# Optimization experiments

Measured on AMD Instinct MI355X. Metric: run time of the kernel, lower is better.

The kernel has to match this reference:

```python
import jax, jax.numpy as jnp
import numpy as np

NUM_HEADS = 16
THETA = 10000.0


def _rope(x):
    # x: [b, h, s, d_k], interleaved-pair RoPE
    s, d = x.shape[-2], x.shape[-1]
    inv_freq = 1.0 / (THETA ** (jnp.arange(0, d, 2, dtype=jnp.float32) / d))  # [d/2]
    ang = jnp.arange(s, dtype=jnp.float32)[:, None] * inv_freq[None, :]       # [s, d/2]
    cos = jnp.repeat(jnp.cos(ang), 2, axis=-1)[None, None]                    # [1,1,s,d]
    sin = jnp.repeat(jnp.sin(ang), 2, axis=-1)[None, None]
    x_even = x[..., 0::2]
    x_odd = x[..., 1::2]
    rot = jnp.stack((-x_odd, x_even), axis=-1).reshape(x.shape)
    return x * cos.astype(x.dtype) + rot * sin.astype(x.dtype)


def setup_inputs() -> dict:
    key = jax.random.key(0)
    ks = jax.random.split(key, 5)
    b, s, d = 4, 2048, 1024
    std = (2.0 / (d + d)) ** 0.5
    return {
        "x": jax.random.normal(ks[0], (b, s, d), dtype=jnp.float32),
        "wq": jax.random.normal(ks[1], (d, d), dtype=jnp.float32) * std,
        "wk": jax.random.normal(ks[2], (d, d), dtype=jnp.float32) * std,
        "wv": jax.random.normal(ks[3], (d, d), dtype=jnp.float32) * std,
        "wo": jax.random.normal(ks[4], (d, d), dtype=jnp.float32) * std,
    }


def reference(x, wq, wk, wv, wo):
    b, s, d_model = x.shape
    h = NUM_HEADS
    d_k = d_model // h

    def proj(w):
        y = jnp.einsum('bsd,od->bso', x, w)
        return y.reshape(b, s, h, d_k).transpose(0, 2, 1, 3)  # [b,h,s,d_k]

    q = _rope(proj(wq))
    k = _rope(proj(wk))
    v = proj(wv)

    scores = jnp.einsum('bhqd,bhkd->bhqk', q, k) / (d_k ** 0.5)
    causal = jnp.tril(jnp.ones((s, s), dtype=bool))[None, None]
    scores = jnp.where(causal, scores, -jnp.inf)
    attn = jax.nn.softmax(scores, axis=-1)
    out = jnp.einsum('bhqk,bhkd->bhqd', attn, v)
    out = out.transpose(0, 2, 1, 3).reshape(b, s, d_model)
    return jnp.einsum('bsd,od->bso', out, wo)
```

## Files before the change

### kernel.cpp

```cpp
#include <hip/hip_runtime.h>
#include <stdint.h>

#define NHEAD  16
#define SEQ    2048
#define DMODEL 1024
#define BATCH  4

typedef __attribute__((ext_vector_type(4))) float f32x4;
typedef __attribute__((ext_vector_type(8))) __bf16 bf16x8;
typedef __attribute__((ext_vector_type(8))) unsigned short u16x8;

__device__ __forceinline__ unsigned short f2bf(float f) {
    unsigned int u = __builtin_bit_cast(unsigned int, f);
    u += 0x7FFFu + ((u >> 16) & 1u);
    return (unsigned short)(u >> 16);
}

__device__ __forceinline__ unsigned int cvt_pk_bf16(float lo, float hi) {
    unsigned int r;
    asm("v_cvt_pk_bf16_f32 %0, %1, %2" : "=v"(r) : "v"(lo), "v"(hi));
    return r;
}

__device__ __forceinline__ void gload_lds16(const void* g, void* l) {
    __builtin_amdgcn_global_load_lds(
        (const __attribute__((address_space(1))) unsigned int*)(uintptr_t)g,
        (__attribute__((address_space(3))) unsigned int*)(uintptr_t)l,
        16, 0, 0);
}

__device__ __forceinline__ bf16x8 lds_frag(const unsigned short* p) {
    return __builtin_bit_cast(bf16x8, *(const u16x8*)p);
}

__device__ __forceinline__ bf16x8 gfrag(const unsigned short* p) {
    return __builtin_bit_cast(bf16x8, *(const u16x8*)p);
}

__global__ __launch_bounds__(256) void cvt_f32_bf16(const float* __restrict__ src,
                                                    unsigned short* __restrict__ dst, int n4) {
    int i = blockIdx.x * 256 + threadIdx.x;
    if (i < n4) {
        float4 v = ((const float4*)src)[i];
        ushort4 o;
        o.x = f2bf(v.x); o.y = f2bf(v.y); o.z = f2bf(v.z); o.w = f2bf(v.w);
        ((ushort4*)dst)[i] = o;
    }
}

__global__ __launch_bounds__(256) void cvt_weights(const float* __restrict__ w0,
                                                   const float* __restrict__ w1,
                                                   const float* __restrict__ w2,
                                                   const float* __restrict__ w3,
                                                   unsigned short* __restrict__ dst) {
    int which = blockIdx.x >> 10;
    int i = (blockIdx.x & 1023) * 256 + threadIdx.x;
    const float* src = which == 0 ? w0 : which == 1 ? w1 : which == 2 ? w2 : w3;
    unsigned short* d = dst + (size_t)which * 1024 * 1024;
    float4 v = ((const float4*)src)[i];
    ushort4 o;
    o.x = f2bf(v.x); o.y = f2bf(v.y); o.z = f2bf(v.z); o.w = f2bf(v.w);
    ((ushort4*)d)[i] = o;
}

__global__ __launch_bounds__(256) void gemm_qkv(const unsigned short* __restrict__ A,
                                                const unsigned short* __restrict__ Wc,
                                                unsigned short* __restrict__ qw,
                                                unsigned short* __restrict__ kw,
                                                unsigned short* __restrict__ vw) {
    __shared__ __align__(16) unsigned short As[2][128 * 64];
    __shared__ __align__(16) unsigned short Bs[2][128 * 64];

    const int tid  = threadIdx.x;
    const int lane = tid & 63;
    const int wid  = tid >> 6;
    const int wm = wid >> 1, wn = wid & 1;
    const int l15 = lane & 15, lg = lane >> 4;

    const int tn = blockIdx.x;
    const int m0 = blockIdx.y * 128, n0 = tn * 128;

    f32x4 acc[4][4];
#pragma unroll
    for (int i = 0; i < 4; i++)
#pragma unroll
        for (int j = 0; j < 4; j++) acc[i][j] = f32x4{0.f, 0.f, 0.f, 0.f};

    const int e0 = tid * 8;
    auto STAGE = [&](int kk, int bufi) {
#pragma unroll
        for (int is = 0; is < 4; ++is) {
            int e = is * 2048 + e0;
            int row = e >> 6, col = e & 63;
            gload_lds16(A  + (size_t)(m0 + row) * 1024 + kk + col, &As[bufi][e]);
            gload_lds16(Wc + (size_t)(n0 + row) * 1024 + kk + col, &Bs[bufi][e]);
        }
    };

    STAGE(0, 0);
    __syncthreads();

    for (int kk = 0; kk < 1024; kk += 64) {
        const int cur = (kk >> 6) & 1;
        if (kk + 64 < 1024) STAGE(kk + 64, cur ^ 1);
#pragma unroll
        for (int ks = 0; ks < 2; ++ks) {
            bf16x8 a[4], b[4];
#pragma unroll
            for (int f = 0; f < 4; f++) {
                a[f] = lds_frag(&As[cur][(wm * 64 + f * 16 + l15) * 64 + ks * 32 + lg * 8]);
                b[f] = lds_frag(&Bs[cur][(wn * 64 + f * 16 + l15) * 64 + ks * 32 + lg * 8]);
            }
#pragma unroll
            for (int i = 0; i < 4; i++)
#pragma unroll
                for (int j = 0; j < 4; j++)
                    acc[i][j] = __builtin_amdgcn_mfma_f32_16x16x32_bf16(a[i], b[j], acc[i][j], 0, 0, 0);
        }
        __syncthreads();
    }

    if (tn >= 16) {
        unsigned short* out = vw;
#pragma unroll
        for (int i = 0; i < 4; i++)
#pragma unroll
            for (int r = 0; r < 4; r++) {
                int m = m0 + wm * 64 + i * 16 + lg * 4 + r;
                int b = m >> 11, s = m & 2047;
#pragma unroll
                for (int j = 0; j < 4; j++) {
                    int n = n0 + wn * 64 + j * 16 + l15;
                    int h = (n >> 6) & 15, dk = n & 63;
                    out[((size_t)(b * NHEAD + h) * 64 + dk) * SEQ + s] = f2bf(acc[i][j][r]);
                }
            }
    } else {
        unsigned short* out = (tn < 8) ? qw : kw;
        const float qscale = (tn < 8) ? 0.18033688011112042f : 1.0f;
        const float L2T = 13.287712379549449f;
        float invf[4];
#pragma unroll
        for (int j = 0; j < 4; j++) {
            int idx = j * 16 + l15;
            int t = idx >> 1;
            invf[j] = exp2f(-((float)(2 * t) * (1.0f / 64.0f)) * L2T);
        }
        const int par = l15 & 1;
#pragma unroll
        for (int i = 0; i < 4; i++)
#pragma unroll
            for (int r = 0; r < 4; r++) {
                int m = m0 + wm * 64 + i * 16 + lg * 4 + r;
                int b = m >> 11, s = m & 2047;
                float fs = (float)s;
#pragma unroll
                for (int j = 0; j < 4; j++) {
                    float v = acc[i][j][r];
                    float other = __shfl_xor(v, 1);
                    float sn, cs;
                    __sincosf(fs * invf[j], &sn, &cs);
                    float y = par ? fmaf(v, cs, other * sn) : fmaf(v, cs, -other * sn);
                    y *= qscale;
                    int n = n0 + wn * 64 + j * 16 + l15;
                    int h = (n >> 6) & 15, dk = n & 63;
                    out[((size_t)(b * NHEAD + h) * SEQ + s) * 64 + dk] = f2bf(y);
                }
            }
    }
}

__global__ __launch_bounds__(256) void gemm_out(const unsigned short* __restrict__ A,
                                                const unsigned short* __restrict__ W,
                                                float* __restrict__ out) {
    __shared__ __align__(16) unsigned short As[2][128 * 64];
    __shared__ __align__(16) unsigned short Bs[2][128 * 64];

    const int tid  = threadIdx.x;
    const int lane = tid & 63;
    const int wid  = tid >> 6;
    const int wm = wid >> 1, wn = wid & 1;
    const int l15 = lane & 15, lg = lane >> 4;

    const int tn = blockIdx.x & 7;
    const int tm = blockIdx.x >> 3;
    const int m0 = tm * 128, n0 = tn * 128;

    f32x4 acc[4][4];
#pragma unroll
    for (int i = 0; i < 4; i++)
#pragma unroll
        for (int j = 0; j < 4; j++) acc[i][j] = f32x4{0.f, 0.f, 0.f, 0.f};

    const int e0 = tid * 8;
    auto STAGE = [&](int kk, int bufi) {
#pragma unroll
        for (int is = 0; is < 4; ++is) {
            int e = is * 2048 + e0;
            int row = e >> 6, col = e & 63;
            gload_lds16(A + (size_t)(m0 + row) * 1024 + kk + col, &As[bufi][e]);
            gload_lds16(W + (size_t)(n0 + row) * 1024 + kk + col, &Bs[bufi][e]);
        }
    };

    STAGE(0, 0);
    __syncthreads();

    for (int kk = 0; kk < 1024; kk += 64) {
        const int cur = (kk >> 6) & 1;
        if (kk + 64 < 1024) STAGE(kk + 64, cur ^ 1);
#pragma unroll
        for (int ks = 0; ks < 2; ++ks) {
            bf16x8 a[4], b[4];
#pragma unroll
            for (int f = 0; f < 4; f++) {
                a[f] = lds_frag(&As[cur][(wm * 64 + f * 16 + l15) * 64 + ks * 32 + lg * 8]);
                b[f] = lds_frag(&Bs[cur][(wn * 64 + f * 16 + l15) * 64 + ks * 32 + lg * 8]);
            }
#pragma unroll
            for (int i = 0; i < 4; i++)
#pragma unroll
                for (int j = 0; j < 4; j++)
                    acc[i][j] = __builtin_amdgcn_mfma_f32_16x16x32_bf16(a[i], b[j], acc[i][j], 0, 0, 0);
        }
        __syncthreads();
    }

#pragma unroll
    for (int i = 0; i < 4; i++)
#pragma unroll
        for (int r = 0; r < 4; r++) {
            int m = m0 + wm * 64 + i * 16 + lg * 4 + r;
            float* orow = out + (size_t)m * 1024 + n0 + wn * 64 + l15;
#pragma unroll
            for (int j = 0; j < 4; j++) orow[j * 16] = acc[i][j][r];
        }
}

__global__ __launch_bounds__(256, 4) void flash_attn(const unsigned short* __restrict__ Qw,
                                                     const unsigned short* __restrict__ Kw,
                                                     const unsigned short* __restrict__ Vw,
                                                     unsigned short* __restrict__ Ow) {
    __shared__ __align__(16) unsigned short Ks[2][64 * 64];
    __shared__ __align__(16) unsigned short Vs[2][64 * 64];
    __shared__ __align__(16) unsigned short Ps[64 * 64];

    const int tid  = threadIdx.x;
    const int lane = tid & 63;
    const int w    = tid >> 6;
    const int l15 = lane & 15, lg = lane >> 4;
    const int l7 = l15 & 7;

    const int logical = (blockIdx.x & 7) * 128 + (blockIdx.x >> 3);
    const int bh = logical >> 4;
    const int p  = logical & 15;
    const int qbB = 31 - p;
    const int ktmax = qbB;

    const unsigned short* Kbh = Kw + (size_t)bh * (SEQ * 64);
    const unsigned short* Vbh = Vw + (size_t)bh * (64 * SEQ);

    const int qrow0 = w * 16;
    const int prow  = qrow0 + l15;

    const unsigned short* QrowA = Qw + (size_t)bh * (SEQ * 64) + (size_t)(p * 64 + prow) * 64;
    const unsigned short* QrowB = Qw + (size_t)bh * (SEQ * 64) + (size_t)(qbB * 64 + prow) * 64;
    bf16x8 qA0 = gfrag(QrowA + lg * 8), qA1 = gfrag(QrowA + 32 + lg * 8);
    bf16x8 qB0 = gfrag(QrowB + lg * 8), qB1 = gfrag(QrowB + 32 + lg * 8);

    auto STAGE = [&](int kt2, int bufi) {
#pragma unroll
        for (int is = 0; is < 2; ++is) {
            int e = (is * 256 + tid) * 8;
            int row = e >> 6, c = (e >> 3) & 7;
            int sc = (c ^ (row & 7)) << 3;
            gload_lds16(Kbh + (size_t)kt2 * 4096 + row * 64 + sc, &Ks[bufi][e]);
            gload_lds16(Vbh + (size_t)row * SEQ + kt2 * 64 + sc, &Vs[bufi][e]);
        }
    };

    STAGE(0, 0);

    f32x4 oaccA[4], oaccB[4];
#pragma unroll
    for (int f = 0; f < 4; f++) { oaccA[f] = f32x4{0.f, 0.f, 0.f, 0.f}; oaccB[f] = f32x4{0.f, 0.f, 0.f, 0.f}; }
    float mA = -3.0e38f, lA = 0.f, mB = -3.0e38f, lB = 0.f;

    unsigned short* pbase = &Ps[prow * 64];
    const unsigned short* prd = &Ps[prow * 64];

    __syncthreads();

    for (int kt = 0; kt <= ktmax; ++kt) {
        const int cur = kt & 1;
        if (kt < ktmax) STAGE(kt + 1, cur ^ 1);

        auto PROC = [&](bf16x8 q0, bf16x8 q1, f32x4* oacc, float& mrun, float& lrun, bool diag) {
            f32x4 st[4];
#pragma unroll
            for (int f = 0; f < 4; f++) st[f] = f32x4{0.f, 0.f, 0.f, 0.f};
            __builtin_amdgcn_s_setprio(1);
#pragma unroll
            for (int ks = 0; ks < 2; ++ks) {
                bf16x8 qk = (ks == 0) ? q0 : q1;
#pragma unroll
                for (int f = 0; f < 4; f++) {
                    bf16x8 kfrag = lds_frag(&Ks[cur][(f * 16 + l15) * 64 + (((ks * 4 + lg) ^ l7) << 3)]);
                    st[f] = __builtin_amdgcn_mfma_f32_16x16x32_bf16(kfrag, qk, st[f], 0, 0, 0);
                }
            }
            __builtin_amdgcn_s_setprio(0);

            if (diag) {
#pragma unroll
                for (int f = 0; f < 4; f++)
#pragma unroll
                    for (int r = 0; r < 4; r++) {
                        int kv = f * 16 + 4 * lg + r;
                        if (kv > prow) st[f][r] = -3.0e38f;
                    }
            }

            float pm = fmaxf(fmaxf(fmaxf(st[0][0], st[0][1]), fmaxf(st[0][2], st[0][3])),
                             fmaxf(fmaxf(st[1][0], st[1][1]), fmaxf(st[1][2], st[1][3])));
            pm = fmaxf(pm, fmaxf(fmaxf(fmaxf(st[2][0], st[2][1]), fmaxf(st[2][2], st[2][3])),
                                 fmaxf(fmaxf(st[3][0], st[3][1]), fmaxf(st[3][2], st[3][3]))));
            pm = fmaxf(pm, __shfl_xor(pm, 16));
            pm = fmaxf(pm, __shfl_xor(pm, 32));

            if (!__all(pm - mrun <= 8.0f)) {
                float mnew = fmaxf(mrun, pm);
                float sc0 = exp2f(mrun - mnew);
                mrun = mnew;
                lrun *= sc0;
#pragma unroll
                for (int r = 0; r < 4; r++) {
                    float so = __shfl(sc0, lg * 4 + r);
#pragma unroll
                    for (int f = 0; f < 4; f++) oacc[f][r] *= so;
                }
            }

            float lsum = 0.f;
#pragma unroll
            for (int f = 0; f < 4; f++)
#pragma unroll
                for (int r = 0; r < 4; r++) {
                    float e = exp2f(st[f][r] - mrun);
                    st[f][r] = e;
                    lsum += e;
                }
            lsum += __shfl_xor(lsum, 16);
            lsum += __shfl_xor(lsum, 32);
            lrun += lsum;

            {
                const int halfoff = (lg & 1) << 2;
                const int cbase = lg >> 1;
#pragma unroll
                for (int f = 0; f < 4; f++) {
                    uint2 pw;
                    pw.x = cvt_pk_bf16(st[f][0], st[f][1]);
                    pw.y = cvt_pk_bf16(st[f][2], st[f][3]);
                    *(uint2*)(pbase + (((2 * f + cbase) ^ l7) << 3) + halfoff) = pw;
                }
            }

            __builtin_amdgcn_s_setprio(1);
#pragma unroll
            for (int ks = 0; ks < 2; ++ks) {
                bf16x8 pa = lds_frag(prd + (((ks * 4 + lg) ^ l7) << 3));
#pragma unroll
                for (int f = 0; f < 4; f++) {
                    bf16x8 vb = lds_frag(&Vs[cur][(f * 16 + l15) * 64 + (((ks * 4 + lg) ^ l7) << 3)]);
                    oacc[f] = __builtin_amdgcn_mfma_f32_16x16x32_bf16(pa, vb, oacc[f], 0, 0, 0);
                }
            }
            __builtin_amdgcn_s_setprio(0);
        };

        if (kt <= p) PROC(qA0, qA1, oaccA, mA, lA, kt == p);
        PROC(qB0, qB1, oaccB, mB, lB, kt == ktmax);

        __syncthreads();
    }

    const int b = bh >> 4, h = bh & 15;
#pragma unroll
    for (int r = 0; r < 4; r++) {
        float lrA = __shfl(lA, lg * 4 + r);
        float invA = 1.0f / lrA;
        int sgA = p * 64 + qrow0 + lg * 4 + r;
        unsigned short* orowA = Ow + ((size_t)(b * SEQ + sgA) * DMODEL) + h * 64 + l15;
#pragma unroll
        for (int f = 0; f < 4; f++) orowA[f * 16] = f2bf(oaccA[f][r] * invA);

        float lrB = __shfl(lB, lg * 4 + r);
        float invB = 1.0f / lrB;
        int sgB = qbB * 64 + qrow0 + lg * 4 + r;
        unsigned short* orowB = Ow + ((size_t)(b * SEQ + sgB) * DMODEL) + h * 64 + l15;
#pragma unroll
        for (int f = 0; f < 4; f++) orowB[f * 16] = f2bf(oaccB[f][r] * invB);
    }
}

extern "C" void kernel_launch(void* const* d_in, const int* in_sizes, int n_in,
                              void* d_out, int out_size, void* d_ws, size_t ws_size,
                              hipStream_t stream) {
    const float* x  = (const float*)d_in[0];
    const float* wq = (const float*)d_in[1];
    const float* wk = (const float*)d_in[2];
    const float* wv = (const float*)d_in[3];
    const float* wo = (const float*)d_in[4];

    unsigned short* ws = (unsigned short*)d_ws;
    const size_t MEL = (size_t)8192 * 1024;
    const size_t WEL = (size_t)1024 * 1024;
    unsigned short* xb  = ws;
    unsigned short* wqb = xb + MEL;
    unsigned short* wob = wqb + 3 * WEL;
    unsigned short* qw  = wob + WEL;
    unsigned short* kw  = qw + MEL;
    unsigned short* vw  = kw + MEL;
    unsigned short* ow  = vw + MEL;

    cvt_f32_bf16<<<8192, 256, 0, stream>>>(x, xb, (int)(MEL / 4));
    cvt_weights<<<4096, 256, 0, stream>>>(wq, wk, wv, wo, wqb);

    gemm_qkv<<<dim3(24, 64), 256, 0, stream>>>(xb, wqb, qw, kw, vw);

    flash_attn<<<1024, 256, 0, stream>>>(qw, kw, vw, ow);

    gemm_out<<<512, 256, 0, stream>>>(ow, wob, (float*)d_out);
}
```

Before: 190.0 us.

## Unify QKV and output GEMMs into 256x128 tile triple-buffered swizzled kernel

Result: slower. 197.4 us (+3.9%).

```diff
diff --git a/kernel.cpp b/kernel.cpp
--- a/kernel.cpp
+++ b/kernel.cpp
@@ -63,22 +63,48 @@
     ((ushort4*)d)[i] = o;
 }
 
-__global__ __launch_bounds__(256) void gemm_qkv(const unsigned short* __restrict__ A,
-                                                const unsigned short* __restrict__ Wc,
-                                                unsigned short* __restrict__ qw,
-                                                unsigned short* __restrict__ kw,
-                                                unsigned short* __restrict__ vw) {
-    __shared__ __align__(16) unsigned short As[2][128 * 64];
-    __shared__ __align__(16) unsigned short Bs[2][128 * 64];
+template <int MODE>
+__global__ __launch_bounds__(512, 1) void gemm256(const unsigned short* __restrict__ A,
+                                                  const unsigned short* __restrict__ Wc,
+                                                  unsigned short* __restrict__ qw,
+                                                  unsigned short* __restrict__ kw,
+                                                  unsigned short* __restrict__ vw,
+                                                  float* __restrict__ fout) {
+    extern __shared__ __align__(16) unsigned short lds[];
+    unsigned short* As = lds;
+    unsigned short* Bs = lds + 3 * 16384;
 
     const int tid  = threadIdx.x;
     const int lane = tid & 63;
     const int wid  = tid >> 6;
     const int wm = wid >> 1, wn = wid & 1;
     const int l15 = lane & 15, lg = lane >> 4;
+    const int l7 = l15 & 7;
 
     const int tn = blockIdx.x;
-    const int m0 = blockIdx.y * 128, n0 = tn * 128;
+    const int m0 = blockIdx.y * 256, n0 = tn * 128;
+
+    auto STAGE_A = [&](int kt, int buf, int is) {
+        int e = (is * 512 + tid) * 8;
+        int row = e >> 6, c = (e >> 3) & 7;
+        gload_lds16(A + (size_t)(m0 + row) * 1024 + kt * 64 + ((c ^ (row & 7)) << 3),
+                    &As[buf * 16384 + e]);
+    };
+    auto STAGE_B = [&](int kt, int buf, int is) {
+        int e = (is * 512 + tid) * 8;
+        int row = e >> 6, c = (e >> 3) & 7;
+        gload_lds16(Wc + (size_t)(n0 + row) * 1024 + kt * 64 + ((c ^ (row & 7)) << 3),
+                    &Bs[buf * 8192 + e]);
+    };
+
+#pragma unroll
+    for (int is = 0; is < 4; ++is) STAGE_A(0, 0, is);
+#pragma unroll
+    for (int is = 0; is < 2; ++is) STAGE_B(0, 0, is);
+#pragma unroll
+    for (int is = 0; is < 4; ++is) STAGE_A(1, 1, is);
+#pragma unroll
+    for (int is = 0; is < 2; ++is) STAGE_B(1, 1, is);
 
     f32x4 acc[4][4];
 #pragma unroll
@@ -86,41 +112,79 @@
 #pragma unroll
         for (int j = 0; j < 4; j++) acc[i][j] = f32x4{0.f, 0.f, 0.f, 0.f};
 
-    const int e0 = tid * 8;
-    auto STAGE = [&](int kk, int bufi) {
-#pragma unroll
-        for (int is = 0; is < 4; ++is) {
-            int e = is * 2048 + e0;
-            int row = e >> 6, col = e & 63;
-            gload_lds16(A  + (size_t)(m0 + row) * 1024 + kk + col, &As[bufi][e]);
-            gload_lds16(Wc + (size_t)(n0 + row) * 1024 + kk + col, &Bs[bufi][e]);
-        }
-    };
-
-    STAGE(0, 0);
-    __syncthreads();
-
-    for (int kk = 0; kk < 1024; kk += 64) {
-        const int cur = (kk >> 6) & 1;
-        if (kk + 64 < 1024) STAGE(kk + 64, cur ^ 1);
-#pragma unroll
-        for (int ks = 0; ks < 2; ++ks) {
+    const int aoff = (wm * 64 + l15) * 64;
+    const int boff = (wn * 64 + l15) * 64;
+    const int c0 = (lg ^ l7) << 3;
+    const int c1 = ((4 + lg) ^ l7) << 3;
+
+    for (int kt = 0; kt < 16; ++kt) {
+        const int buf  = kt % 3;
+        const int buf2 = (kt + 2) % 3;
+        const unsigned short* Ab = As + buf * 16384;
+        const unsigned short* Bb = Bs + buf * 8192;
+
+        if (kt < 15) asm volatile("s_waitcnt vmcnt(6)" ::: "memory");
+        else         asm volatile("s_waitcnt vmcnt(0)" ::: "memory");
+        __builtin_amdgcn_sched_barrier(0);
+        __builtin_amdgcn_s_barrier();
+
+        if (kt + 2 < 16) {
+            STAGE_A(kt + 2, buf2, 0);
+            STAGE_A(kt + 2, buf2, 1);
+            STAGE_A(kt + 2, buf2, 2);
+        }
+        {
             bf16x8 a[4], b[4];
 #pragma unroll
-            for (int f = 0; f < 4; f++) {
-                a[f] = lds_frag(&As[cur][(wm * 64 + f * 16 + l15) * 64 + ks * 32 + lg * 8]);
-                b[f] = lds_frag(&Bs[cur][(wn * 64 + f * 16 + l15) * 64 + ks * 32 + lg * 8]);
-            }
+            for (int i = 0; i < 4; i++) a[i] = lds_frag(Ab + aoff + i * 1024 + c0);
+#pragma unroll
+            for (int n = 0; n < 4; n++) b[n] = lds_frag(Bb + boff + n * 1024 + c0);
+            asm volatile("s_waitcnt lgkmcnt(0)" ::: "memory");
+            __builtin_amdgcn_sched_barrier(0);
+            __builtin_amdgcn_s_setprio(1);
 #pragma unroll
             for (int i = 0; i < 4; i++)
 #pragma unroll
-                for (int j = 0; j < 4; j++)
-                    acc[i][j] = __builtin_amdgcn_mfma_f32_16x16x32_bf16(a[i], b[j], acc[i][j], 0, 0, 0);
-        }
-        __syncthreads();
+                for (int n = 0; n < 4; n++)
+                    acc[i][n] = __builtin_amdgcn_mfma_f32_16x16x32_bf16(a[i], b[n], acc[i][n], 0, 0, 0);
+            __builtin_amdgcn_s_setprio(0);
+        }
+
+        if (kt + 2 < 16) {
+            STAGE_A(kt + 2, buf2, 3);
+            STAGE_B(kt + 2, buf2, 0);
+            STAGE_B(kt + 2, buf2, 1);
+        }
+        {
+            bf16x8 a[4], b[4];
+#pragma unroll
+            for (int i = 0; i < 4; i++) a[i] = lds_frag(Ab + aoff + i * 1024 + c1);
+#pragma unroll
+            for (int n = 0; n < 4; n++) b[n] = lds_frag(Bb + boff + n * 1024 + c1);
+            asm volatile("s_waitcnt lgkmcnt(0)" ::: "memory");
+            __builtin_amdgcn_sched_barrier(0);
+            __builtin_amdgcn_s_setprio(1);
+#pragma unroll
+            for (int i = 0; i < 4; i++)
+#pragma unroll
+                for (int n = 0; n < 4; n++)
+                    acc[i][n] = __builtin_amdgcn_mfma_f32_16x16x32_bf16(a[i], b[n], acc[i][n], 0, 0, 0);
+            __builtin_amdgcn_s_setprio(0);
+        }
     }
 
-    if (tn >= 16) {
+    if (MODE == 1) {
+        float* out = fout;
+#pragma unroll
+        for (int i = 0; i < 4; i++)
+#pragma unroll
+            for (int r = 0; r < 4; r++) {
+                int m = m0 + wm * 64 + i * 16 + lg * 4 + r;
+                float* orow = out + (size_t)m * 1024 + n0 + wn * 64 + l15;
+#pragma unroll
+                for (int j = 0; j < 4; j++) orow[j * 16] = acc[i][j][r];
+            }
+    } else if (tn >= 16) {
         unsigned short* out = vw;
 #pragma unroll
         for (int i = 0; i < 4; i++)
@@ -170,73 +234,6 @@
     }
 }
 
-__global__ __launch_bounds__(256) void gemm_out(const unsigned short* __restrict__ A,
-                                                const unsigned short* __restrict__ W,
-                                                float* __restrict__ out) {
-    __shared__ __align__(16) unsigned short As[2][128 * 64];
-    __shared__ __align__(16) unsigned short Bs[2][128 * 64];
-
-    const int tid  = threadIdx.x;
-    const int lane = tid & 63;
-    const int wid  = tid >> 6;
-    const int wm = wid >> 1, wn = wid & 1;
-    const int l15 = lane & 15, lg = lane >> 4;
-
-    const int tn = blockIdx.x & 7;
-    const int tm = blockIdx.x >> 3;
-    const int m0 = tm * 128, n0 = tn * 128;
-
-    f32x4 acc[4][4];
-#pragma unroll
-    for (int i = 0; i < 4; i++)
-#pragma unroll
-        for (int j = 0; j < 4; j++) acc[i][j] = f32x4{0.f, 0.f, 0.f, 0.f};
-
-    const int e0 = tid * 8;
-    auto STAGE = [&](int kk, int bufi) {
-#pragma unroll
-        for (int is = 0; is < 4; ++is) {
-            int e = is * 2048 + e0;
-            int row = e >> 6, col = e & 63;
-            gload_lds16(A + (size_t)(m0 + row) * 1024 + kk + col, &As[bufi][e]);
-            gload_lds16(W + (size_t)(n0 + row) * 1024 + kk + col, &Bs[bufi][e]);
-        }
-    };
-
-    STAGE(0, 0);
-    __syncthreads();
-
-    for (int kk = 0; kk < 1024; kk += 64) {
-        const int cur = (kk >> 6) & 1;
-        if (kk + 64 < 1024) STAGE(kk + 64, cur ^ 1);
-#pragma unroll
-        for (int ks = 0; ks < 2; ++ks) {
-            bf16x8 a[4], b[4];
-#pragma unroll
-            for (int f = 0; f < 4; f++) {
-                a[f] = lds_frag(&As[cur][(wm * 64 + f * 16 + l15) * 64 + ks * 32 + lg * 8]);
-                b[f] = lds_frag(&Bs[cur][(wn * 64 + f * 16 + l15) * 64 + ks * 32 + lg * 8]);
-            }
-#pragma unroll
-            for (int i = 0; i < 4; i++)
-#pragma unroll
-                for (int j = 0; j < 4; j++)
-                    acc[i][j] = __builtin_amdgcn_mfma_f32_16x16x32_bf16(a[i], b[j], acc[i][j], 0, 0, 0);
-        }
-        __syncthreads();
-    }
-
-#pragma unroll
-    for (int i = 0; i < 4; i++)
-#pragma unroll
-        for (int r = 0; r < 4; r++) {
-            int m = m0 + wm * 64 + i * 16 + lg * 4 + r;
-            float* orow = out + (size_t)m * 1024 + n0 + wn * 64 + l15;
-#pragma unroll
-            for (int j = 0; j < 4; j++) orow[j * 16] = acc[i][j][r];
-        }
-}
-
 __global__ __launch_bounds__(256, 4) void flash_attn(const unsigned short* __restrict__ Qw,
                                                      const unsigned short* __restrict__ Kw,
                                                      const unsigned short* __restrict__ Vw,
@@ -424,12 +421,18 @@
     unsigned short* vw  = kw + MEL;
     unsigned short* ow  = vw + MEL;
 
+    const int GEMM_LDS = (3 * 16384 + 3 * 8192) * 2;
+    (void)hipFuncSetAttribute((const void*)gemm256<0>,
+                              hipFuncAttributeMaxDynamicSharedMemorySize, GEMM_LDS);
+    (void)hipFuncSetAttribute((const void*)gemm256<1>,
+                              hipFuncAttributeMaxDynamicSharedMemorySize, GEMM_LDS);
+
     cvt_f32_bf16<<<8192, 256, 0, stream>>>(x, xb, (int)(MEL / 4));
     cvt_weights<<<4096, 256, 0, stream>>>(wq, wk, wv, wo, wqb);
 
-    gemm_qkv<<<dim3(24, 64), 256, 0, stream>>>(xb, wqb, qw, kw, vw);
+    gemm256<0><<<dim3(24, 32), 512, GEMM_LDS, stream>>>(xb, wqb, qw, kw, vw, nullptr);
 
     flash_attn<<<1024, 256, 0, stream>>>(qw, kw, vw, ow);
 
-    gemm_out<<<512, 256, 0, stream>>>(ow, wob, (float*)d_out);
-}
+    gemm256<1><<<dim3(8, 32), 512, GEMM_LDS, stream>>>(ow, wob, nullptr, nullptr, nullptr, (float*)d_out);
+}
```
